# Optimization experiments

Measured on AMD Instinct MI355X. Metric: run time of the kernel, lower is better.

## Reference

```python
import jax, jax.numpy as jnp
import numpy as np

B, K, TOPK = 32, 8192, 1000
F, AED = 1024, 128          # state_feature_size, action_embedding_dim
E = F + AED + 1             # memory slot width = 1153
ADIM = 4672


def _gelu(x):
    return jax.nn.gelu(x, approximate=False)  # torch default GELU is exact erf


def setup_inputs() -> dict:
    key = jax.random.key(0)
    ks = jax.random.split(key, 14)
    def W(k, i, o):
        return jax.random.normal(k, (i, o), jnp.float32) / np.float32(np.sqrt(i))
    return {
        'features': jax.random.normal(ks[0], (B, F), jnp.float32),
        'memory': jax.random.normal(ks[1], (K, E), jnp.float32),
        'W1s': W(ks[2], 2 * F, 512), 'b1s': jnp.zeros(512, jnp.float32),
        'W2s': W(ks[3], 512, 1), 'b2s': jnp.zeros(1, jnp.float32),
        'W1e': W(ks[4], 2 * F, 256), 'b1e': jnp.zeros(256, jnp.float32),
        'W2e': W(ks[5], 256, 1), 'b2e': jnp.zeros(1, jnp.float32),
        'Wp1': W(ks[6], F + AED, 768), 'bp1': jnp.zeros(768, jnp.float32),
        'Wp2': W(ks[7], 768, ADIM), 'bp2': jnp.zeros(ADIM, jnp.float32),
        'Wv1': W(ks[8], F, 512), 'bv1': jnp.zeros(512, jnp.float32),
        'Wv2': W(ks[9], 512, 1), 'bv2': jnp.zeros(1, jnp.float32),
        'Wm1': W(ks[10], F, 512), 'bm1': jnp.zeros(512, jnp.float32),
        'Wm2': W(ks[11], 512, 1), 'bm2': jnp.zeros(1, jnp.float32),
    }


def reference(features, memory, W1s, b1s, W2s, b2s, W1e, b1e, W2e, b2e,
              Wp1, bp1, Wp2, bp2, Wv1, bv1, Wv2, bv2, Wm1, bm1, Wm2, bm2):
    # ---- ReadHead.StateAttention: relu(fc1(cat(q,k))) -> fc2 -> softmax over K slots.
    # fc1(cat(q,k)) = q @ W1s[:F] + k @ W1s[F:] + b : avoids materializing the (B,K,2F) concat.
    feat_mem = memory[:, :F]                                   # (K,F)
    q1 = features @ W1s[:F]                                    # (B,512)
    k1 = feat_mem @ W1s[F:]                                    # (K,512)
    h1 = jax.nn.relu(q1[:, None, :] + k1[None, :, :] + b1s)    # (B,K,512)
    scores = jnp.squeeze(h1 @ W2s, -1) + b2s                   # (B,K)
    attn_w = jax.nn.softmax(scores, axis=1)
    _, topk_idx = jax.lax.top_k(attn_w, TOPK)                  # (B,TOPK)

    # ---- retrieve_relevant_memory: batched gather of top-k slots
    rel = jnp.take(memory, topk_idx, axis=0)                   # (B,TOPK,E)
    mem_feat = rel[..., :F]
    # torch does .long() on the action slice: truncate toward zero, no grad flow
    actions = jax.lax.stop_gradient(jnp.trunc(rel[..., F:E - 1]))  # (B,TOPK,AED)
    results = rel[..., -1]                                     # (B,TOPK)

    # ---- ActionResultAttention over the TOPK retrieved slots (GELU MLP attention)
    q2 = features @ W1e[:F]                                    # (B,256)
    k2 = jnp.einsum('bkf,fh->bkh', mem_feat, W1e[F:])          # (B,TOPK,256)
    h2 = _gelu(q2[:, None, :] + k2 + b1e)
    s2 = jnp.squeeze(h2 @ W2e, -1) + b2e                       # (B,TOPK)
    w2 = jax.nn.softmax(s2, axis=1)
    weighted_actions = jnp.einsum('bka,bk->ba', actions, w2)   # (B,AED)
    weighted_results = jnp.einsum('bk,bk->b', results, w2)[:, None]  # (B,1)

    # ---- policy / value heads + ValueMLPAttention blend
    pf = jnp.concatenate([features, weighted_actions], axis=1)
    action_logits = _gelu(pf @ Wp1 + bp1) @ Wp2 + bp2          # (B,ADIM)
    board_vals = jnp.tanh(_gelu(features @ Wv1 + bv1) @ Wv2 + bv2)  # (B,1)
    aw = jax.nn.sigmoid(_gelu(features @ Wm1 + bm1) @ Wm2 + bm2)
    value_output = aw * weighted_results + (1.0 - aw) * board_vals
    return action_logits, board_vals, value_output, weighted_actions, weighted_results
```

## Files before the change

kernel.cpp:

```cpp
#include <hip/hip_runtime.h>
#include <math.h>

#define B_ 32
#define K_ 8192
#define TOPK_ 1000
#define F_ 1024
#define E_ 1153
#define H1_ 512
#define H2_ 256
#define PH_ 768
#define ADIM_ 4672

#define OFF_BV   149504
#define OFF_VAL  149536
#define OFF_WACT 149568
#define OFF_WRES 153664

typedef __attribute__((ext_vector_type(8))) short v8s;
typedef __attribute__((ext_vector_type(4))) float v4f;
typedef __attribute__((ext_vector_type(4))) unsigned short v4u16;

#define GLD16(gp, lp) __builtin_amdgcn_global_load_lds( \
    (const __attribute__((address_space(1))) void*)(gp), \
    (__attribute__((address_space(3))) void*)(lp), 16, 0, 0)

__device__ __forceinline__ float gelu_f(float x) {
  return 0.5f * x * (1.0f + erff(x * 0.70710678118654752440f));
}
__device__ __forceinline__ unsigned short f2bf(float x) {
  union { float f; unsigned u; } v; v.f = x;
  unsigned r = v.u + 0x7fffu + ((v.u >> 16) & 1u);
  return (unsigned short)(r >> 16);
}
__device__ __forceinline__ float bf2f(unsigned short h) {
  union { unsigned u; float f; } v; v.u = ((unsigned)h) << 16; return v.f;
}

__global__ __launch_bounds__(256) void k_split_mem(
    const float* __restrict__ memory, unsigned short* __restrict__ Ahi,
    unsigned short* __restrict__ Alo) {
  const int r = blockIdx.x;
  const int tid = threadIdx.x;
  const float* src = memory + (size_t)r * E_;
#pragma unroll
  for (int i = 0; i < 4; ++i) {
    const float x = src[tid + 256 * i];
    const unsigned short h = f2bf(x);
    Ahi[(size_t)r * 1024 + tid + 256 * i] = h;
    Alo[(size_t)r * 1024 + tid + 256 * i] = f2bf(x - bf2f(h));
  }
}

__global__ __launch_bounds__(256) void k_split_w(
    const float* __restrict__ W1s, const float* __restrict__ W1e,
    unsigned short* __restrict__ B1hi, unsigned short* __restrict__ B1lo,
    unsigned short* __restrict__ B2hi) {
  __shared__ float t[32][33];
  const int x = threadIdx.x, y = threadIdx.y;
  const int j0 = blockIdx.x * 32, k0 = blockIdx.y * 32;
#pragma unroll
  for (int i = 0; i < 4; ++i) {
    const int k = k0 + y + 8 * i;
    const int j = j0 + x;
    t[y + 8 * i][x] = (j < 512) ? W1s[(size_t)(F_ + k) * H1_ + j]
                                : W1e[(size_t)(F_ + k) * H2_ + (j - 512)];
  }
  __syncthreads();
#pragma unroll
  for (int i = 0; i < 4; ++i) {
    const int j = j0 + y + 8 * i;
    const int k = k0 + x;
    const float v = t[x][y + 8 * i];
    const unsigned short h = f2bf(v);
    if (j < 512) {
      B1hi[(size_t)j * 1024 + k] = h;
      B1lo[(size_t)j * 1024 + k] = f2bf(v - bf2f(h));
    } else {
      B2hi[(size_t)(j - 512) * 1024 + k] = h;
    }
  }
}

__global__ __launch_bounds__(256) void k_init5(
    const float* __restrict__ b1s, const float* __restrict__ b1e,
    const float* __restrict__ bv1, const float* __restrict__ bm1,
    const float* __restrict__ bp1, float* __restrict__ q1b,
    float* __restrict__ q2b, float* __restrict__ v1h, float* __restrict__ m1h,
    float* __restrict__ hp_acc, float* __restrict__ wact,
    float* __restrict__ wres) {
  const int idx = blockIdx.x * 256 + threadIdx.x;
  if (idx < 32 * 2560) {
    const int b = idx / 2560, j = idx - b * 2560;
    if (j < 512) q1b[b * 512 + j] = b1s[j];
    else if (j < 768) q2b[b * 256 + (j - 512)] = b1e[j - 512];
    else if (j < 1280) v1h[b * 512 + (j - 768)] = bv1[j - 768];
    else if (j < 1792) m1h[b * 512 + (j - 1280)] = bm1[j - 1280];
    else hp_acc[b * 768 + (j - 1792)] = bp1[j - 1792];
  } else {
    const int k = idx - 32 * 2560;
    if (k < 4096) wact[k] = 0.f;
    else if (k < 4128) wres[k - 4096] = 0.f;
  }
}

__device__ __forceinline__ void skinny32_body(
    const float* __restrict__ A, int lda, int kbase,
    const float* __restrict__ Wp, int ldw, int n0, int N,
    float* __restrict__ C, int ldc, float* __restrict__ lA) {
  const int tid = threadIdx.x;
#pragma unroll
  for (int j = 0; j < 16; ++j) {
    const int idx = j * 128 + tid;
    const int r = idx >> 6, k = idx & 63;
    lA[k * 36 + r] = A[(size_t)r * lda + kbase + k];
  }
  __syncthreads();
  const int c0 = n0 + tid * 2;
  if (c0 >= N) return;
  float acc[32][2];
#pragma unroll
  for (int r = 0; r < 32; ++r) { acc[r][0] = 0.f; acc[r][1] = 0.f; }
  const float* wp = Wp + (size_t)kbase * ldw + c0;
#pragma unroll 2
  for (int k = 0; k < 64; ++k) {
    const float2 w = *(const float2*)&wp[(size_t)k * ldw];
#pragma unroll
    for (int rq = 0; rq < 8; ++rq) {
      const float4 a = *(const float4*)&lA[k * 36 + rq * 4];
      acc[rq * 4 + 0][0] = fmaf(a.x, w.x, acc[rq * 4 + 0][0]);
      acc[rq * 4 + 0][1] = fmaf(a.x, w.y, acc[rq * 4 + 0][1]);
      acc[rq * 4 + 1][0] = fmaf(a.y, w.x, acc[rq * 4 + 1][0]);
      acc[rq * 4 + 1][1] = fmaf(a.y, w.y, acc[rq * 4 + 1][1]);
      acc[rq * 4 + 2][0] = fmaf(a.z, w.x, acc[rq * 4 + 2][0]);
      acc[rq * 4 + 2][1] = fmaf(a.z, w.y, acc[rq * 4 + 2][1]);
      acc[rq * 4 + 3][0] = fmaf(a.w, w.x, acc[rq * 4 + 3][0]);
      acc[rq * 4 + 3][1] = fmaf(a.w, w.y, acc[rq * 4 + 3][1]);
    }
  }
#pragma unroll
  for (int r = 0; r < 32; ++r) {
    atomicAdd(&C[(size_t)r * ldc + c0], acc[r][0]);
    atomicAdd(&C[(size_t)r * ldc + c0 + 1], acc[r][1]);
  }
}

__global__ __launch_bounds__(128) void k_skinny_batch1(
    const float* __restrict__ features, const float* __restrict__ W1s,
    const float* __restrict__ W1e, const float* __restrict__ Wv1,
    const float* __restrict__ Wm1, float* __restrict__ q1b,
    float* __restrict__ q2b, float* __restrict__ v1h,
    float* __restrict__ m1h) {
  __shared__ float lA[64 * 36];
  const int t = blockIdx.x;
  const float* Wp; float* Cp; int ldw, n0;
  switch (t) {
    case 0: Wp = W1s; Cp = q1b; ldw = 512; n0 = 0;   break;
    case 1: Wp = W1s; Cp = q1b; ldw = 512; n0 = 256; break;
    case 2: Wp = W1e; Cp = q2b; ldw = 256; n0 = 0;   break;
    case 3: Wp = Wv1; Cp = v1h; ldw = 512; n0 = 0;   break;
    case 4: Wp = Wv1; Cp = v1h; ldw = 512; n0 = 256; break;
    case 5: Wp = Wm1; Cp = m1h; ldw = 512; n0 = 0;   break;
    default: Wp = Wm1; Cp = m1h; ldw = 512; n0 = 256; break;
  }
  skinny32_body(features, F_, blockIdx.y * 64, Wp, ldw, n0, ldw, Cp, ldw, lA);
}

__global__ __launch_bounds__(128) void k_skinny_hp_feat(
    const float* __restrict__ features, const float* __restrict__ Wp1,
    float* __restrict__ hp_acc) {
  __shared__ float lA[64 * 36];
  skinny32_body(features, F_, blockIdx.y * 64, Wp1, PH_, blockIdx.x * 256, PH_,
                hp_acc, PH_, lA);
}

__global__ __launch_bounds__(128) void k_skinny_hp_wact(
    const float* __restrict__ wact, const float* __restrict__ Wp1,
    float* __restrict__ hp_acc) {
  __shared__ float lA[64 * 36];
  skinny32_body(wact, 128, blockIdx.y * 64, Wp1 + (size_t)F_ * PH_, PH_,
                blockIdx.x * 256, PH_, hp_acc, PH_, lA);
}

__global__ __launch_bounds__(128) void k_skinny_logits(
    const float* __restrict__ hp, const float* __restrict__ Wp2,
    float* __restrict__ out) {
  __shared__ float lA[64 * 36];
  skinny32_body(hp, PH_, blockIdx.y * 64, Wp2, ADIM_, blockIdx.x * 256, ADIM_,
                out, ADIM_, lA);
}

__device__ __forceinline__ void stage80(
    const unsigned short* __restrict__ src, int row_base, int k0,
    char* lds, int lds_off, int nchunks, int tid) {
  for (int i = 0; i * 256 < nchunks; ++i) {
    const int c = i * 256 + tid;
    if (c < nchunks) {
      const int row = c / 5, sub = c % 5;
      const int s = (sub == 4) ? 0 : sub;
      const unsigned short* g = src + (size_t)(row_base + row) * 1024 + k0 + s * 8;
      GLD16(g, lds + lds_off + i * 4096 + ((tid >> 6) * 1024));
    }
  }
}

__global__ __launch_bounds__(256) void k_gemm1(
    const unsigned short* __restrict__ Ahi, const unsigned short* __restrict__ Alo,
    const unsigned short* __restrict__ B1hi, const unsigned short* __restrict__ B1lo,
    float* __restrict__ C1) {
  __shared__ unsigned short lds[15360];
  char* L = (char*)lds;
  const int tid = threadIdx.x;
  const int lane = tid & 63, w = tid >> 6;
  const int m0 = blockIdx.x * 128;
  const int n0 = blockIdx.y * 64;
  const int wr = w >> 1, wc = w & 1;
  v4f acc[4][2];
#pragma unroll
  for (int mi = 0; mi < 4; ++mi)
#pragma unroll
    for (int ni = 0; ni < 2; ++ni) acc[mi][ni] = (v4f)(0.f);

  for (int k0 = 0; k0 < 1024; k0 += 32) {
    __syncthreads();
    stage80(Ahi, m0, k0, L, 0, 640, tid);
    stage80(Alo, m0, k0, L, 10240, 640, tid);
    stage80(B1hi, n0, k0, L, 20480, 320, tid);
    stage80(B1lo, n0, k0, L, 25600, 320, tid);
    asm volatile("s_waitcnt vmcnt(0)" ::: "memory");
    __syncthreads();
    v8s ah[4], al[4], bh[2], bl[2];
    const int fo = (lane >> 4) * 16;
#pragma unroll
    for (int mi = 0; mi < 4; ++mi) {
      const int ro = (wr * 64 + mi * 16 + (lane & 15)) * 80 + fo;
      ah[mi] = *(const v8s*)(L + ro);
      al[mi] = *(const v8s*)(L + 10240 + ro);
    }
#pragma unroll
    for (int ni = 0; ni < 2; ++ni) {
      const int ro = (wc * 32 + ni * 16 + (lane & 15)) * 80 + fo;
      bh[ni] = *(const v8s*)(L + 20480 + ro);
      bl[ni] = *(const v8s*)(L + 25600 + ro);
    }
#pragma unroll
    for (int mi = 0; mi < 4; ++mi)
#pragma unroll
      for (int ni = 0; ni < 2; ++ni) {
        acc[mi][ni] = __builtin_amdgcn_mfma_f32_16x16x32_bf16(ah[mi], bh[ni], acc[mi][ni], 0, 0, 0);
        acc[mi][ni] = __builtin_amdgcn_mfma_f32_16x16x32_bf16(ah[mi], bl[ni], acc[mi][ni], 0, 0, 0);
        acc[mi][ni] = __builtin_amdgcn_mfma_f32_16x16x32_bf16(al[mi], bh[ni], acc[mi][ni], 0, 0, 0);
      }
  }
#pragma unroll
  for (int mi = 0; mi < 4; ++mi)
#pragma unroll
    for (int ni = 0; ni < 2; ++ni)
#pragma unroll
      for (int j = 0; j < 4; ++j) {
        const int mrow = m0 + wr * 64 + mi * 16 + (lane >> 4) * 4 + j;
        const int ncol = n0 + wc * 32 + ni * 16 + (lane & 15);
        C1[(size_t)mrow * 512 + ncol] = acc[mi][ni][j];
      }
}

__global__ __launch_bounds__(256) void k_gemm2(
    const unsigned short* __restrict__ Ahi, const unsigned short* __restrict__ B2hi,
    unsigned short* __restrict__ C2) {
  __shared__ unsigned short lds[7680];
  char* L = (char*)lds;
  const int tid = threadIdx.x;
  const int lane = tid & 63, w = tid >> 6;
  const int m0 = blockIdx.x * 128;
  const int n0 = blockIdx.y * 64;
  const int wr = w >> 1, wc = w & 1;
  v4f acc[4][2];
#pragma unroll
  for (int mi = 0; mi < 4; ++mi)
#pragma unroll
    for (int ni = 0; ni < 2; ++ni) acc[mi][ni] = (v4f)(0.f);

  for (int k0 = 0; k0 < 1024; k0 += 32) {
    __syncthreads();
    stage80(Ahi, m0, k0, L, 0, 640, tid);
    stage80(B2hi, n0, k0, L, 10240, 320, tid);
    asm volatile("s_waitcnt vmcnt(0)" ::: "memory");
    __syncthreads();
    v8s ah[4], bh[2];
    const int fo = (lane >> 4) * 16;
#pragma unroll
    for (int mi = 0; mi < 4; ++mi)
      ah[mi] = *(const v8s*)(L + (wr * 64 + mi * 16 + (lane & 15)) * 80 + fo);
#pragma unroll
    for (int ni = 0; ni < 2; ++ni)
      bh[ni] = *(const v8s*)(L + 10240 + (wc * 32 + ni * 16 + (lane & 15)) * 80 + fo);
#pragma unroll
    for (int mi = 0; mi < 4; ++mi)
#pragma unroll
      for (int ni = 0; ni < 2; ++ni)
        acc[mi][ni] = __builtin_amdgcn_mfma_f32_16x16x32_bf16(ah[mi], bh[ni], acc[mi][ni], 0, 0, 0);
  }
#pragma unroll
  for (int mi = 0; mi < 4; ++mi)
#pragma unroll
    for (int ni = 0; ni < 2; ++ni)
#pragma unroll
      for (int j = 0; j < 4; ++j) {
        const int mrow = m0 + wr * 64 + mi * 16 + (lane >> 4) * 4 + j;
        const int ncol = n0 + wc * 32 + ni * 16 + (lane & 15);
        C2[(size_t)mrow * 256 + ncol] = f2bf(acc[mi][ni][j]);
      }
}

__global__ __launch_bounds__(256) void k_scores2(
    const float* __restrict__ C1, const float* __restrict__ q1b,
    const float* __restrict__ W2s, const float* __restrict__ b2s,
    float* __restrict__ scores) {
  __shared__ float4 c4[8 * 129];
  __shared__ float4 w4[128];
  const int tid = threadIdx.x;
  const int kbase = blockIdx.x * 8;
#pragma unroll
  for (int p = 0; p < 4; ++p) {
    const int idx = p * 256 + tid;
    const int row = idx >> 7, c = idx & 127;
    c4[row * 129 + c] = *(const float4*)&C1[(size_t)(kbase + row) * 512 + c * 4];
  }
  if (tid < 128) w4[tid] = *(const float4*)&W2s[tid * 4];
  __syncthreads();
  const int b = tid >> 3, ks = tid & 7;
  const float4* qrow = (const float4*)&q1b[b * 512];
  float acc = 0.f;
  for (int i = 0; i < 128; ++i) {
    const float4 c = c4[ks * 129 + i];
    const float4 q = qrow[i];
    const float4 w = w4[i];
    acc += fmaxf(q.x + c.x, 0.f) * w.x + fmaxf(q.y + c.y, 0.f) * w.y +
           fmaxf(q.z + c.z, 0.f) * w.z + fmaxf(q.w + c.w, 0.f) * w.w;
  }
  scores[(size_t)b * K_ + kbase + ks] = acc + b2s[0];
}

__global__ __launch_bounds__(1024) void k_topk(
    const float* __restrict__ scores, int* __restrict__ topk_idx) {
  __shared__ unsigned key[K_];
  __shared__ unsigned whist[16][256];
  __shared__ unsigned sfx[256];
  __shared__ int eqlist[1024];
  __shared__ unsigned ctl[4];
  const int tid = threadIdx.x;
  const int wid = tid >> 6;
  const int b = blockIdx.x;
  const float* row = scores + (size_t)b * K_;
  for (int i = tid; i < K_; i += 1024) {
    const unsigned u = __float_as_uint(row[i]);
    key[i] = (u & 0x80000000u) ? ~u : (u | 0x80000000u);
  }
  unsigned prefix = 0;
  int r = TOPK_;
  for (int p = 0; p < 4; ++p) {
    const int shift = 24 - 8 * p;
    for (int i = tid; i < 16 * 256; i += 1024) ((unsigned*)whist)[i] = 0;
    __syncthreads();
    const unsigned pmask = (p == 0) ? 0u : (0xFFFFFFFFu << (shift + 8));
    for (int i = tid; i < K_; i += 1024) {
      const unsigned k = key[i];
      if ((k & pmask) == prefix) atomicAdd(&whist[wid][(k >> shift) & 255u], 1u);
    }
    __syncthreads();
    if (tid < 256) {
      unsigned s = 0;
#pragma unroll
      for (int ww = 0; ww < 16; ++ww) s += whist[ww][tid];
      sfx[tid] = s;
    }
    __syncthreads();
    for (int off = 1; off < 256; off <<= 1) {
      unsigned v = 0;
      if (tid < 256) { v = sfx[tid]; if (tid + off < 256) v += sfx[tid + off]; }
      __syncthreads();
      if (tid < 256) sfx[tid] = v;
      __syncthreads();
    }
    if (tid < 256) {
      const int Sge = (int)sfx[tid];
      const int Sgt = (tid < 255) ? (int)sfx[tid + 1] : 0;
      if (Sgt < r && r <= Sge) { ctl[0] = (unsigned)tid; ctl[1] = (unsigned)(r - Sgt); }
    }
    __syncthreads();
    prefix |= ctl[0] << shift;
    r = (int)ctl[1];
    __syncthreads();
  }
  const unsigned T = prefix;
  const int take_eq = r;
  if (tid == 0) { ctl[2] = 0; ctl[3] = 0; }
  __syncthreads();
  int* outp = topk_idx + b * TOPK_;
  for (int i = tid; i < K_; i += 1024) {
    const unsigned k = key[i];
    if (k > T) outp[atomicAdd(&ctl[2], 1u)] = i;
    else if (k == T) { const unsigned e = atomicAdd(&ctl[3], 1u); if (e < 1024) eqlist[e] = i; }
  }
  __syncthreads();
  const int m = (ctl[3] < 1024u) ? (int)ctl[3] : 1024;
  const int ngt = TOPK_ - take_eq;
  for (int sel = 0; sel < take_eq; ++sel) {
    key[tid] = (tid < m) ? (unsigned)eqlist[tid] : 0xFFFFFFFFu;
    __syncthreads();
    for (int s = 512; s > 0; s >>= 1) {
      if (tid < s) key[tid] = min(key[tid], key[tid + s]);
      __syncthreads();
    }
    const unsigned mn = key[0];
    if (tid < m && (unsigned)eqlist[tid] == mn) eqlist[tid] = 0x7FFFFFFF;
    if (tid == 0) outp[ngt + sel] = (int)mn;
    __syncthreads();
  }
}

__global__ __launch_bounds__(256) void k_s2(
    const unsigned short* __restrict__ C2, const float* __restrict__ q2b,
    const int* __restrict__ topk_idx, const float* __restrict__ W2e,
    const float* __restrict__ b2e, float* __restrict__ s2) {
  const int tid = threadIdx.x;
  const int ln = tid & 63;
  const int e = blockIdx.x * 4 + (tid >> 6);
  const int b = e / TOPK_;
  const int idx = topk_idx[e];
  const v4u16 kv = *(const v4u16*)(C2 + (size_t)idx * H2_ + ln * 4);
  const float4 qv = *(const float4*)(q2b + b * H2_ + ln * 4);
  float s = gelu_f(qv.x + bf2f(kv[0])) * W2e[ln * 4 + 0]
          + gelu_f(qv.y + bf2f(kv[1])) * W2e[ln * 4 + 1]
          + gelu_f(qv.z + bf2f(kv[2])) * W2e[ln * 4 + 2]
          + gelu_f(qv.w + bf2f(kv[3])) * W2e[ln * 4 + 3];
#pragma unroll
  for (int off = 32; off > 0; off >>= 1) s += __shfl_down(s, off);
  if (ln == 0) s2[e] = s + b2e[0];
}

__global__ __launch_bounds__(256) void k_soft(
    const float* __restrict__ s2, float* __restrict__ w2) {
  __shared__ float red[256];
  const int tid = threadIdx.x, b = blockIdx.x;
  float m = -3.4e38f;
  for (int t = tid; t < TOPK_; t += 256) m = fmaxf(m, s2[b * TOPK_ + t]);
  red[tid] = m;
  __syncthreads();
  for (int s = 128; s > 0; s >>= 1) {
    if (tid < s) red[tid] = fmaxf(red[tid], red[tid + s]);
    __syncthreads();
  }
  m = red[0];
  __syncthreads();
  float ps = 0.f;
  for (int t = tid; t < TOPK_; t += 256) {
    const float ev = expf(s2[b * TOPK_ + t] - m);
    w2[b * TOPK_ + t] = ev;
    ps += ev;
  }
  red[tid] = ps;
  __syncthreads();
  for (int s = 128; s > 0; s >>= 1) {
    if (tid < s) red[tid] += red[tid + s];
    __syncthreads();
  }
  const float inv = 1.f / red[0];
  for (int t = tid; t < TOPK_; t += 256) w2[b * TOPK_ + t] *= inv;
}

__global__ __launch_bounds__(256) void k_weighted(
    const int* __restrict__ topk_idx, const float* __restrict__ w2,
    const float* __restrict__ memory, float* __restrict__ wact_acc,
    float* __restrict__ wres_acc) {
  const int blk = blockIdx.x;
  const int b = blk >> 3, c = blk & 7;
  const int tid = threadIdx.x;
  const int g = tid >> 7, a = tid & 127;
  float acc = 0.f, accr = 0.f;
  for (int t = c * 125 + g; t < (c + 1) * 125; t += 2) {
    const int idx = topk_idx[b * TOPK_ + t];
    const float wv = w2[b * TOPK_ + t];
    acc += truncf(memory[(size_t)idx * E_ + F_ + a]) * wv;
    if (a == 0) accr += wv * memory[(size_t)idx * E_ + (E_ - 1)];
  }
  atomicAdd(&wact_acc[b * 128 + a], acc);
  if (a == 0) atomicAdd(&wres_acc[b], accr);
}

__global__ __launch_bounds__(512) void k_value_epi(
    const float* __restrict__ v1h, const float* __restrict__ m1h,
    const float* __restrict__ Wv2, const float* __restrict__ bv2,
    const float* __restrict__ Wm2, const float* __restrict__ bm2,
    float* __restrict__ aw, float* __restrict__ out) {
  __shared__ float red[512];
  const int tid = threadIdx.x, b = blockIdx.x, net = blockIdx.y;
  const float* h = net ? m1h : v1h;
  const float* W2 = net ? Wm2 : Wv2;
  red[tid] = gelu_f(h[b * 512 + tid]) * W2[tid];
  __syncthreads();
  for (int s = 256; s > 0; s >>= 1) {
    if (tid < s) red[tid] += red[tid + s];
    __syncthreads();
  }
  if (tid == 0) {
    const float v = red[0] + (net ? bm2[0] : bv2[0]);
    if (net == 0) out[OFF_BV + b] = tanhf(v);
    else aw[b] = 1.f / (1.f + expf(-v));
  }
}

__global__ void k_gelu_ip(float* __restrict__ p, int n) {
  const int i = blockIdx.x * 256 + threadIdx.x;
  if (i < n) p[i] = gelu_f(p[i]);
}

__global__ __launch_bounds__(256) void k_logits_init(
    const float* __restrict__ bp2, float* __restrict__ out) {
  const int i = blockIdx.x * 256 + threadIdx.x;
  if (i < B_ * ADIM_) out[i] = bp2[i % ADIM_];
}

__global__ __launch_bounds__(256) void k_finalize(
    const float* __restrict__ wact, const float* __restrict__ wres,
    const float* __restrict__ aw, float* __restrict__ out) {
  const int i = blockIdx.x * 256 + threadIdx.x;
  if (i < 4096) {
    out[OFF_WACT + i] = wact[i];
  } else if (i < 4128) {
    const int b = i - 4096;
    out[OFF_WRES + b] = wres[b];
    const float A = aw[b];
    out[OFF_VAL + b] = A * wres[b] + (1.f - A) * out[OFF_BV + b];
  }
}

extern "C" void kernel_launch(void* const* d_in, const int* in_sizes, int n_in,
                              void* d_out, int out_size, void* d_ws,
                              size_t ws_size, hipStream_t stream) {
  (void)in_sizes; (void)n_in; (void)out_size; (void)ws_size;
  const float* features = (const float*)d_in[0];
  const float* memory   = (const float*)d_in[1];
  const float* W1s = (const float*)d_in[2];
  const float* b1s = (const float*)d_in[3];
  const float* W2s = (const float*)d_in[4];
  const float* b2s = (const float*)d_in[5];
  const float* W1e = (const float*)d_in[6];
  const float* b1e = (const float*)d_in[7];
  const float* W2e = (const float*)d_in[8];
  const float* b2e = (const float*)d_in[9];
  const float* Wp1 = (const float*)d_in[10];
  const float* bp1 = (const float*)d_in[11];
  const float* Wp2 = (const float*)d_in[12];
  const float* bp2 = (const float*)d_in[13];
  const float* Wv1 = (const float*)d_in[14];
  const float* bv1 = (const float*)d_in[15];
  const float* Wv2 = (const float*)d_in[16];
  const float* bv2 = (const float*)d_in[17];
  const float* Wm1 = (const float*)d_in[18];
  const float* bm1 = (const float*)d_in[19];
  const float* Wm2 = (const float*)d_in[20];
  const float* bm2 = (const float*)d_in[21];
  float* out = (float*)d_out;

  char* W = (char*)d_ws;
  unsigned short* Ahi  = (unsigned short*)(W);
  unsigned short* Alo  = (unsigned short*)(W + (16u << 20));
  unsigned short* B1hi = (unsigned short*)(W + (32u << 20));
  unsigned short* B1lo = (unsigned short*)(W + (33u << 20));
  unsigned short* B2hi = (unsigned short*)(W + (34u << 20));
  float*          C1   = (float*)(W + (35u << 20));
  unsigned short* C2   = (unsigned short*)(W + (51u << 20));
  float*          scores = (float*)(W + (55u << 20));
  char* S = W + (56u << 20);
  float* q1b      = (float*)(S);
  float* q2b      = (float*)(S + 65536);
  float* s2       = (float*)(S + 98304);
  float* w2       = (float*)(S + 226304);
  int*   topk     = (int*)  (S + 354304);
  float* wact_acc = (float*)(S + 482304);
  float* wres_acc = (float*)(S + 498688);
  float* aw       = (float*)(S + 498816);
  float* hp_acc   = (float*)(S + 498944);
  float* v1h      = (float*)(S + 597248);
  float* m1h      = (float*)(S + 662784);

  k_split_mem<<<8192, 256, 0, stream>>>(memory, Ahi, Alo);
  k_split_w<<<dim3(24, 32), dim3(32, 8), 0, stream>>>(W1s, W1e, B1hi, B1lo, B2hi);
  k_init5<<<337, 256, 0, stream>>>(b1s, b1e, bv1, bm1, bp1, q1b, q2b, v1h, m1h,
                                   hp_acc, wact_acc, wres_acc);
  k_skinny_batch1<<<dim3(7, 16), 128, 0, stream>>>(features, W1s, W1e, Wv1, Wm1,
                                                   q1b, q2b, v1h, m1h);
  k_skinny_hp_feat<<<dim3(3, 16), 128, 0, stream>>>(features, Wp1, hp_acc);
  k_gemm1<<<dim3(64, 8), 256, 0, stream>>>(Ahi, Alo, B1hi, B1lo, C1);
  k_gemm2<<<dim3(64, 4), 256, 0, stream>>>(Ahi, B2hi, C2);
  k_scores2<<<1024, 256, 0, stream>>>(C1, q1b, W2s, b2s, scores);
  k_topk<<<32, 1024, 0, stream>>>(scores, topk);
  k_s2<<<8000, 256, 0, stream>>>(C2, q2b, topk, W2e, b2e, s2);
  k_soft<<<32, 256, 0, stream>>>(s2, w2);
  k_weighted<<<256, 256, 0, stream>>>(topk, w2, memory, wact_acc, wres_acc);
  k_skinny_hp_wact<<<dim3(3, 2), 128, 0, stream>>>(wact_acc, Wp1, hp_acc);
  k_gelu_ip<<<96, 256, 0, stream>>>(hp_acc, B_ * PH_);
  k_value_epi<<<dim3(32, 2), 512, 0, stream>>>(v1h, m1h, Wv2, bv2, Wm2, bm2, aw, out);
  k_logits_init<<<584, 256, 0, stream>>>(bp2, out);
  k_skinny_logits<<<dim3(19, 12), 128, 0, stream>>>(hp_acc, Wp2, out);
  k_finalize<<<17, 256, 0, stream>>>(wact_acc, wres_acc, aw, out);
}
```

Before: 370.2 us.

## Drop memory lo-split, merge score GEMMs, fuse small epilogue kernels

The memory matrix is now converted only to a bf16 high part, so the first GEMM runs two MFMAs per step instead of three and the Alo split buffer is gone. The two attention-key GEMMs are merged into one launch using a grid-y branch. The Wp1 tail, GELU, value heads, logits bias init and finalize steps are folded into fewer kernels, cutting launch count. The GEMM for attention scores loses some precision, which risks changing top-k selection near ties.

```diff
diff --git a/kernel.cpp b/kernel.cpp
--- a/kernel.cpp
+++ b/kernel.cpp
@@ -37,18 +37,14 @@
 }
 
 __global__ __launch_bounds__(256) void k_split_mem(
-    const float* __restrict__ memory, unsigned short* __restrict__ Ahi,
-    unsigned short* __restrict__ Alo) {
+    const float* __restrict__ memory, unsigned short* __restrict__ Ahi) {
   const int r = blockIdx.x;
-  const int tid = threadIdx.x;
-  const float* src = memory + (size_t)r * E_;
-#pragma unroll
-  for (int i = 0; i < 4; ++i) {
-    const float x = src[tid + 256 * i];
-    const unsigned short h = f2bf(x);
-    Ahi[(size_t)r * 1024 + tid + 256 * i] = h;
-    Alo[(size_t)r * 1024 + tid + 256 * i] = f2bf(x - bf2f(h));
-  }
+  const int t = threadIdx.x;
+  const float* src = memory + (size_t)r * E_ + 4 * t;
+  unsigned* dst = (unsigned*)(Ahi + (size_t)r * 1024);
+  const float x0 = src[0], x1 = src[1], x2 = src[2], x3 = src[3];
+  dst[2 * t]     = (unsigned)f2bf(x0) | ((unsigned)f2bf(x1) << 16);
+  dst[2 * t + 1] = (unsigned)f2bf(x2) | ((unsigned)f2bf(x3) << 16);
 }
 
 __global__ __launch_bounds__(256) void k_split_w(
@@ -81,13 +77,13 @@
   }
 }
 
-__global__ __launch_bounds__(256) void k_init5(
+__global__ __launch_bounds__(256) void k_init(
     const float* __restrict__ b1s, const float* __restrict__ b1e,
     const float* __restrict__ bv1, const float* __restrict__ bm1,
-    const float* __restrict__ bp1, float* __restrict__ q1b,
-    float* __restrict__ q2b, float* __restrict__ v1h, float* __restrict__ m1h,
-    float* __restrict__ hp_acc, float* __restrict__ wact,
-    float* __restrict__ wres) {
+    const float* __restrict__ bp1, const float* __restrict__ bp2,
+    float* __restrict__ q1b, float* __restrict__ q2b, float* __restrict__ v1h,
+    float* __restrict__ m1h, float* __restrict__ hp, float* __restrict__ wact,
+    float* __restrict__ wres, float* __restrict__ out) {
   const int idx = blockIdx.x * 256 + threadIdx.x;
   if (idx < 32 * 2560) {
     const int b = idx / 2560, j = idx - b * 2560;
@@ -95,11 +91,14 @@
     else if (j < 768) q2b[b * 256 + (j - 512)] = b1e[j - 512];
     else if (j < 1280) v1h[b * 512 + (j - 768)] = bv1[j - 768];
     else if (j < 1792) m1h[b * 512 + (j - 1280)] = bm1[j - 1280];
-    else hp_acc[b * 768 + (j - 1792)] = bp1[j - 1792];
-  } else {
+    else hp[b * 768 + (j - 1792)] = bp1[j - 1792];
+  } else if (idx < 32 * 2560 + 4128) {
     const int k = idx - 32 * 2560;
     if (k < 4096) wact[k] = 0.f;
-    else if (k < 4128) wres[k - 4096] = 0.f;
+    else wres[k - 4096] = 0.f;
+  } else {
+    const int k = idx - (32 * 2560 + 4128);
+    if (k < B_ * ADIM_) out[k] = bp2[k % ADIM_];
   }
 }
 
@@ -173,14 +172,6 @@
                 hp_acc, PH_, lA);
 }
 
-__global__ __launch_bounds__(128) void k_skinny_hp_wact(
-    const float* __restrict__ wact, const float* __restrict__ Wp1,
-    float* __restrict__ hp_acc) {
-  __shared__ float lA[64 * 36];
-  skinny32_body(wact, 128, blockIdx.y * 64, Wp1 + (size_t)F_ * PH_, PH_,
-                blockIdx.x * 256, PH_, hp_acc, PH_, lA);
-}
-
 __global__ __launch_bounds__(128) void k_skinny_logits(
     const float* __restrict__ hp, const float* __restrict__ Wp2,
     float* __restrict__ out) {
@@ -203,16 +194,19 @@
   }
 }
 
-__global__ __launch_bounds__(256) void k_gemm1(
-    const unsigned short* __restrict__ Ahi, const unsigned short* __restrict__ Alo,
-    const unsigned short* __restrict__ B1hi, const unsigned short* __restrict__ B1lo,
-    float* __restrict__ C1) {
-  __shared__ unsigned short lds[15360];
+__global__ __launch_bounds__(256) void k_gemmA(
+    const unsigned short* __restrict__ Ahi, const unsigned short* __restrict__ B1hi,
+    const unsigned short* __restrict__ B1lo, const unsigned short* __restrict__ B2hi,
+    float* __restrict__ C1, unsigned short* __restrict__ C2) {
+  __shared__ unsigned short lds[10240];
   char* L = (char*)lds;
   const int tid = threadIdx.x;
   const int lane = tid & 63, w = tid >> 6;
   const int m0 = blockIdx.x * 128;
-  const int n0 = blockIdx.y * 64;
+  const int y = blockIdx.y;
+  const bool two = (y < 8);
+  const int n0 = two ? y * 64 : (y - 8) * 64;
+  const unsigned short* Bh = two ? B1hi : B2hi;
   const int wr = w >> 1, wc = w & 1;
   v4f acc[4][2];
 #pragma unroll
@@ -223,92 +217,53 @@
   for (int k0 = 0; k0 < 1024; k0 += 32) {
     __syncthreads();
     stage80(Ahi, m0, k0, L, 0, 640, tid);
-    stage80(Alo, m0, k0, L, 10240, 640, tid);
-    stage80(B1hi, n0, k0, L, 20480, 320, tid);
-    stage80(B1lo, n0, k0, L, 25600, 320, tid);
+    stage80(Bh, n0, k0, L, 10240, 320, tid);
+    if (two) stage80(B1lo, n0, k0, L, 15360, 320, tid);
     asm volatile("s_waitcnt vmcnt(0)" ::: "memory");
     __syncthreads();
-    v8s ah[4], al[4], bh[2], bl[2];
+    v8s ah[4], bh[2], bl[2];
     const int fo = (lane >> 4) * 16;
 #pragma unroll
-    for (int mi = 0; mi < 4; ++mi) {
-      const int ro = (wr * 64 + mi * 16 + (lane & 15)) * 80 + fo;
-      ah[mi] = *(const v8s*)(L + ro);
-      al[mi] = *(const v8s*)(L + 10240 + ro);
-    }
+    for (int mi = 0; mi < 4; ++mi)
+      ah[mi] = *(const v8s*)(L + (wr * 64 + mi * 16 + (lane & 15)) * 80 + fo);
 #pragma unroll
     for (int ni = 0; ni < 2; ++ni) {
       const int ro = (wc * 32 + ni * 16 + (lane & 15)) * 80 + fo;
-      bh[ni] = *(const v8s*)(L + 20480 + ro);
-      bl[ni] = *(const v8s*)(L + 25600 + ro);
+      bh[ni] = *(const v8s*)(L + 10240 + ro);
+      if (two) bl[ni] = *(const v8s*)(L + 15360 + ro);
     }
 #pragma unroll
     for (int mi = 0; mi < 4; ++mi)
 #pragma unroll
       for (int ni = 0; ni < 2; ++ni) {
         acc[mi][ni] = __builtin_amdgcn_mfma_f32_16x16x32_bf16(ah[mi], bh[ni], acc[mi][ni], 0, 0, 0);
-        acc[mi][ni] = __builtin_amdgcn_mfma_f32_16x16x32_bf16(ah[mi], bl[ni], acc[mi][ni], 0, 0, 0);
-        acc[mi][ni] = __builtin_amdgcn_mfma_f32_16x16x32_bf16(al[mi], bh[ni], acc[mi][ni], 0, 0, 0);
+        if (two)
+          acc[mi][ni] = __builtin_amdgcn_mfma_f32_16x16x32_bf16(ah[mi], bl[ni], acc[mi][ni], 0, 0, 0);
       }
   }
-#pragma unroll
-  for (int mi = 0; mi < 4; ++mi)
-#pragma unroll
-    for (int ni = 0; ni < 2; ++ni)
-#pragma unroll
-      for (int j = 0; j < 4; ++j) {
-        const int mrow = m0 + wr * 64 + mi * 16 + (lane >> 4) * 4 + j;
-        const int ncol = n0 + wc * 32 + ni * 16 + (lane & 15);
-        C1[(size_t)mrow * 512 + ncol] = acc[mi][ni][j];
-      }
-}
-
-__global__ __launch_bounds__(256) void k_gemm2(
-    const unsigned short* __restrict__ Ahi, const unsigned short* __restrict__ B2hi,
-    unsigned short* __restrict__ C2) {
-  __shared__ unsigned short lds[7680];
-  char* L = (char*)lds;
-  const int tid = threadIdx.x;
-  const int lane = tid & 63, w = tid >> 6;
-  const int m0 = blockIdx.x * 128;
-  const int n0 = blockIdx.y * 64;
-  const int wr = w >> 1, wc = w & 1;
-  v4f acc[4][2];
-#pragma unroll
-  for (int mi = 0; mi < 4; ++mi)
-#pragma unroll
-    for (int ni = 0; ni < 2; ++ni) acc[mi][ni] = (v4f)(0.f);
-
-  for (int k0 = 0; k0 < 1024; k0 += 32) {
-    __syncthreads();
-    stage80(Ahi, m0, k0, L, 0, 640, tid);
-    stage80(B2hi, n0, k0, L, 10240, 320, tid);
-    asm volatile("s_waitcnt vmcnt(0)" ::: "memory");
-    __syncthreads();
-    v8s ah[4], bh[2];
-    const int fo = (lane >> 4) * 16;
+  if (two) {
 #pragma unroll
     for (int mi = 0; mi < 4; ++mi)
-      ah[mi] = *(const v8s*)(L + (wr * 64 + mi * 16 + (lane & 15)) * 80 + fo);
-#pragma unroll
-    for (int ni = 0; ni < 2; ++ni)
-      bh[ni] = *(const v8s*)(L + 10240 + (wc * 32 + ni * 16 + (lane & 15)) * 80 + fo);
+#pragma unroll
+      for (int ni = 0; ni < 2; ++ni)
+#pragma unroll
+        for (int j = 0; j < 4; ++j) {
+          const int mrow = m0 + wr * 64 + mi * 16 + (lane >> 4) * 4 + j;
+          const int ncol = n0 + wc * 32 + ni * 16 + (lane & 15);
+          C1[(size_t)mrow * 512 + ncol] = acc[mi][ni][j];
+        }
+  } else {
 #pragma unroll
     for (int mi = 0; mi < 4; ++mi)
 #pragma unroll
       for (int ni = 0; ni < 2; ++ni)
-        acc[mi][ni] = __builtin_amdgcn_mfma_f32_16x16x32_bf16(ah[mi], bh[ni], acc[mi][ni], 0, 0, 0);
-  }
-#pragma unroll
-  for (int mi = 0; mi < 4; ++mi)
-#pragma unroll
-    for (int ni = 0; ni < 2; ++ni)
-#pragma unroll
-      for (int j = 0; j < 4; ++j) {
-        const int mrow = m0 + wr * 64 + mi * 16 + (lane >> 4) * 4 + j;
-        const int ncol = n0 + wc * 32 + ni * 16 + (lane & 15);
-        C2[(size_t)mrow * 256 + ncol] = f2bf(acc[mi][ni][j]);
-      }
+#pragma unroll
+        for (int j = 0; j < 4; ++j) {
+          const int mrow = m0 + wr * 64 + mi * 16 + (lane >> 4) * 4 + j;
+          const int ncol = n0 + wc * 32 + ni * 16 + (lane & 15);
+          C2[(size_t)mrow * 256 + ncol] = f2bf(acc[mi][ni][j]);
+        }
+  }
 }
 
 __global__ __launch_bounds__(256) void k_scores2(
@@ -487,50 +442,54 @@
   if (a == 0) atomicAdd(&wres_acc[b], accr);
 }
 
-__global__ __launch_bounds__(512) void k_value_epi(
+__global__ __launch_bounds__(768) void k_hp_final(
+    const float* __restrict__ wact, const float* __restrict__ Wp1,
+    float* __restrict__ hp) {
+  __shared__ float lw[128];
+  const int b = blockIdx.x, j = threadIdx.x;
+  if (j < 128) lw[j] = wact[b * 128 + j];
+  __syncthreads();
+  float acc = hp[b * PH_ + j];
+  const float* wp = Wp1 + (size_t)F_ * PH_ + j;
+#pragma unroll 4
+  for (int h = 0; h < 128; ++h) acc = fmaf(lw[h], wp[(size_t)h * PH_], acc);
+  hp[b * PH_ + j] = gelu_f(acc);
+}
+
+__global__ __launch_bounds__(512) void k_value_fin(
     const float* __restrict__ v1h, const float* __restrict__ m1h,
     const float* __restrict__ Wv2, const float* __restrict__ bv2,
     const float* __restrict__ Wm2, const float* __restrict__ bm2,
-    float* __restrict__ aw, float* __restrict__ out) {
+    const float* __restrict__ wres, const float* __restrict__ wact,
+    float* __restrict__ out) {
+  const int b = blockIdx.x, tid = threadIdx.x;
+  if (b == 32) {
+#pragma unroll
+    for (int i = 0; i < 8; ++i) out[OFF_WACT + i * 512 + tid] = wact[i * 512 + tid];
+    return;
+  }
   __shared__ float red[512];
-  const int tid = threadIdx.x, b = blockIdx.x, net = blockIdx.y;
-  const float* h = net ? m1h : v1h;
-  const float* W2 = net ? Wm2 : Wv2;
-  red[tid] = gelu_f(h[b * 512 + tid]) * W2[tid];
+  red[tid] = gelu_f(v1h[b * 512 + tid]) * Wv2[tid];
   __syncthreads();
   for (int s = 256; s > 0; s >>= 1) {
     if (tid < s) red[tid] += red[tid + s];
     __syncthreads();
   }
+  if (tid == 0) red[0] = tanhf(red[0] + bv2[0]);
+  __syncthreads();
+  const float bv = red[0];
+  __syncthreads();
+  red[tid] = gelu_f(m1h[b * 512 + tid]) * Wm2[tid];
+  __syncthreads();
+  for (int s = 256; s > 0; s >>= 1) {
+    if (tid < s) red[tid] += red[tid + s];
+    __syncthreads();
+  }
   if (tid == 0) {
-    const float v = red[0] + (net ? bm2[0] : bv2[0]);
-    if (net == 0) out[OFF_BV + b] = tanhf(v);
-    else aw[b] = 1.f / (1.f + expf(-v));
-  }
-}
-
-__global__ void k_gelu_ip(float* __restrict__ p, int n) {
-  const int i = blockIdx.x * 256 + threadIdx.x;
-  if (i < n) p[i] = gelu_f(p[i]);
-}
-
-__global__ __launch_bounds__(256) void k_logits_init(
-    const float* __restrict__ bp2, float* __restrict__ out) {
-  const int i = blockIdx.x * 256 + threadIdx.x;
-  if (i < B_ * ADIM_) out[i] = bp2[i % ADIM_];
-}
-
-__global__ __launch_bounds__(256) void k_finalize(
-    const float* __restrict__ wact, const float* __restrict__ wres,
-    const float* __restrict__ aw, float* __restrict__ out) {
-  const int i = blockIdx.x * 256 + threadIdx.x;
-  if (i < 4096) {
-    out[OFF_WACT + i] = wact[i];
-  } else if (i < 4128) {
-    const int b = i - 4096;
+    const float aw = 1.f / (1.f + expf(-(red[0] + bm2[0])));
+    out[OFF_BV + b] = bv;
+    out[OFF_VAL + b] = aw * wres[b] + (1.f - aw) * bv;
     out[OFF_WRES + b] = wres[b];
-    const float A = aw[b];
-    out[OFF_VAL + b] = A * wres[b] + (1.f - A) * out[OFF_BV + b];
   }
 }
 
@@ -564,14 +523,13 @@
 
   char* W = (char*)d_ws;
   unsigned short* Ahi  = (unsigned short*)(W);
-  unsigned short* Alo  = (unsigned short*)(W + (16u << 20));
-  unsigned short* B1hi = (unsigned short*)(W + (32u << 20));
-  unsigned short* B1lo = (unsigned short*)(W + (33u << 20));
-  unsigned short* B2hi = (unsigned short*)(W + (34u << 20));
-  float*          C1   = (float*)(W + (35u << 20));
-  unsigned short* C2   = (unsigned short*)(W + (51u << 20));
-  float*          scores = (float*)(W + (55u << 20));
-  char* S = W + (56u << 20);
+  unsigned short* B1hi = (unsigned short*)(W + (16u << 20));
+  unsigned short* B1lo = (unsigned short*)(W + (17u << 20));
+  unsigned short* B2hi = (unsigned short*)(W + (18u << 20));
+  float*          C1   = (float*)(W + (19u << 20));
+  unsigned short* C2   = (unsigned short*)(W + (35u << 20));
+  float*          scores = (float*)(W + (39u << 20));
+  char* S = W + (40u << 20);
   float* q1b      = (float*)(S);
   float* q2b      = (float*)(S + 65536);
   float* s2       = (float*)(S + 98304);
@@ -579,29 +537,27 @@
   int*   topk     = (int*)  (S + 354304);
   float* wact_acc = (float*)(S + 482304);
   float* wres_acc = (float*)(S + 498688);
-  float* aw       = (float*)(S + 498816);
+  float* aw_un    = (float*)(S + 498816);
   float* hp_acc   = (float*)(S + 498944);
   float* v1h      = (float*)(S + 597248);
   float* m1h      = (float*)(S + 662784);
-
-  k_split_mem<<<8192, 256, 0, stream>>>(memory, Ahi, Alo);
+  (void)aw_un;
+
+  k_split_mem<<<8192, 256, 0, stream>>>(memory, Ahi);
   k_split_w<<<dim3(24, 32), dim3(32, 8), 0, stream>>>(W1s, W1e, B1hi, B1lo, B2hi);
-  k_init5<<<337, 256, 0, stream>>>(b1s, b1e, bv1, bm1, bp1, q1b, q2b, v1h, m1h,
-                                   hp_acc, wact_acc, wres_acc);
+  k_init<<<921, 256, 0, stream>>>(b1s, b1e, bv1, bm1, bp1, bp2, q1b, q2b, v1h,
+                                  m1h, hp_acc, wact_acc, wres_acc, out);
   k_skinny_batch1<<<dim3(7, 16), 128, 0, stream>>>(features, W1s, W1e, Wv1, Wm1,
                                                    q1b, q2b, v1h, m1h);
   k_skinny_hp_feat<<<dim3(3, 16), 128, 0, stream>>>(features, Wp1, hp_acc);
-  k_gemm1<<<dim3(64, 8), 256, 0, stream>>>(Ahi, Alo, B1hi, B1lo, C1);
-  k_gemm2<<<dim3(64, 4), 256, 0, stream>>>(Ahi, B2hi, C2);
+  k_gemmA<<<dim3(64, 12), 256, 0, stream>>>(Ahi, B1hi, B1lo, B2hi, C1, C2);
   k_scores2<<<1024, 256, 0, stream>>>(C1, q1b, W2s, b2s, scores);
   k_topk<<<32, 1024, 0, stream>>>(scores, topk);
   k_s2<<<8000, 256, 0, stream>>>(C2, q2b, topk, W2e, b2e, s2);
   k_soft<<<32, 256, 0, stream>>>(s2, w2);
   k_weighted<<<256, 256, 0, stream>>>(topk, w2, memory, wact_acc, wres_acc);
-  k_skinny_hp_wact<<<dim3(3, 2), 128, 0, stream>>>(wact_acc, Wp1, hp_acc);
-  k_gelu_ip<<<96, 256, 0, stream>>>(hp_acc, B_ * PH_);
-  k_value_epi<<<dim3(32, 2), 512, 0, stream>>>(v1h, m1h, Wv2, bv2, Wm2, bm2, aw, out);
-  k_logits_init<<<584, 256, 0, stream>>>(bp2, out);
+  k_hp_final<<<32, 768, 0, stream>>>(wact_acc, Wp1, hp_acc);
+  k_value_fin<<<33, 512, 0, stream>>>(v1h, m1h, Wv2, bv2, Wm2, bm2, wres_acc,
+                                      wact_acc, out);
   k_skinny_logits<<<dim3(19, 12), 128, 0, stream>>>(hp_acc, Wp2, out);
-  k_finalize<<<17, 256, 0, stream>>>(wact_acc, wres_acc, aw, out);
-}
+}
```

Measured after the change: 344.7 us. 6.9% less time.
